# Kernel optimization log

Hardware: AMD Instinct MI355X
Metric: run time of the kernel (lower is better)

Reference implementation:

```python
import jax, jax.numpy as jnp
import numpy as np

BETA = 0.25
NUM_EMB = 8192
EMB_DIM = 256


def setup_inputs() -> dict:
    key = jax.random.key(0)
    k1, k2 = jax.random.split(key)
    z = jax.random.normal(k1, (32, 32, 32, EMB_DIM), dtype=jnp.float32)
    # codebook init: uniform in [-1/K, 1/K], stored as [D, K] like the TF layer
    embeddings = jax.random.uniform(
        k2, (EMB_DIM, NUM_EMB), dtype=jnp.float32,
        minval=-1.0 / NUM_EMB, maxval=1.0 / NUM_EMB)
    return {"z": z, "embeddings": embeddings}


def reference(z, embeddings):
    # inference path (training falsy): no EMA updates
    z_flat = z.reshape(-1, EMB_DIM)  # [N, D]
    # squared euclidean distances [N, K]
    distances = (jnp.sum(z_flat * z_flat, axis=1, keepdims=True)
                 + jnp.sum(embeddings * embeddings, axis=0)
                 - 2.0 * (z_flat @ embeddings))
    encoding_indices = jnp.argmin(distances, axis=1)  # [N] int
    quantized = embeddings.T[encoding_indices].reshape(z.shape)

    commitment_loss = BETA * jnp.mean((jax.lax.stop_gradient(quantized) - z) ** 2)
    # straight-through estimator
    quantized_st = z + jax.lax.stop_gradient(quantized - z)

    # avg one-hot probs via scatter-add (avoids materializing [N, K] one-hot)
    n_tokens = z_flat.shape[0]
    counts = jnp.zeros((NUM_EMB,), dtype=jnp.float32).at[encoding_indices].add(1.0)
    avg_probs = counts / n_tokens
    perplexity = jnp.exp(-jnp.sum(avg_probs * jnp.log(avg_probs + 1e-10)))

    return (quantized_st, encoding_indices, 0, commitment_loss, perplexity)
```

## Files before the change

### kernel.cpp

```cpp
#include <hip/hip_runtime.h>
#include <math.h>
#include <stdint.h>


#define N_TOK   32768
#define DIM     256
#define K_EMB   8192

#define WS_S       0
#define WS_E2      131072
#define WS_PVAL    163840
#define WS_PIDX    425984
#define WS_CNT     688128
#define WS_PART    720896
#define WS_ZT      851968
#define WS_END_ZT  34406400
#define WS_ET      34406400
#define WS_END_ET  42795008

__device__ __forceinline__ void gload_lds16(const float* g, float* l) {
  __builtin_amdgcn_global_load_lds(
      (const __attribute__((address_space(1))) void*)g,
      (__attribute__((address_space(3))) void*)l, 16, 0, 0);
}

__global__ void k_sumz(const float* __restrict__ z, float* __restrict__ S) {
  int t = blockIdx.x * blockDim.x + threadIdx.x;
  const float4* zp = (const float4*)(z + (size_t)t * DIM);
  float s = 0.0f;
  #pragma unroll 4
  for (int g = 0; g < DIM / 4; ++g) {
    float4 v = zp[g];
    s = __fadd_rn(s, __fmul_rn(v.x, v.x));
    s = __fadd_rn(s, __fmul_rn(v.y, v.y));
    s = __fadd_rn(s, __fmul_rn(v.z, v.z));
    s = __fadd_rn(s, __fmul_rn(v.w, v.w));
  }
  S[t] = s;
}

__global__ void k_sume(const float* __restrict__ E, float* __restrict__ e2) {
  __shared__ float part[4][64];
  int c  = threadIdx.x & 63;
  int dq = threadIdx.x >> 6;
  int col = blockIdx.x * 64 + c;
  float s = 0.0f;
  #pragma unroll 4
  for (int d = dq * 64; d < dq * 64 + 64; ++d) {
    float v = E[(size_t)d * K_EMB + col];
    s = __fadd_rn(s, __fmul_rn(v, v));
  }
  part[dq][c] = s;
  __syncthreads();
  if (threadIdx.x < 64)
    e2[blockIdx.x * 64 + threadIdx.x] =
        __fadd_rn(__fadd_rn(part[0][threadIdx.x], part[1][threadIdx.x]),
                  __fadd_rn(part[2][threadIdx.x], part[3][threadIdx.x]));
}

__global__ void k_transpose_z(const float* __restrict__ z, float* __restrict__ zT) {
  __shared__ float tile[32][33];
  int n0 = blockIdx.x * 32, d0 = blockIdx.y * 32;
  int lx = threadIdx.x, ly = threadIdx.y;
  #pragma unroll
  for (int r = 0; r < 32; r += 8)
    tile[ly + r][lx] = z[(size_t)(n0 + ly + r) * DIM + d0 + lx];
  __syncthreads();
  #pragma unroll
  for (int r = 0; r < 32; r += 8)
    zT[(size_t)(d0 + ly + r) * N_TOK + n0 + lx] = tile[lx][ly + r];
}

__global__ void k_transpose_e(const float* __restrict__ E, float* __restrict__ ET) {
  __shared__ float tile[32][33];
  int k0 = blockIdx.x * 32, d0 = blockIdx.y * 32;
  int lx = threadIdx.x, ly = threadIdx.y;
  #pragma unroll
  for (int r = 0; r < 32; r += 8)
    tile[ly + r][lx] = E[(size_t)(d0 + ly + r) * K_EMB + k0 + lx];
  __syncthreads();
  #pragma unroll
  for (int r = 0; r < 32; r += 8)
    ET[(size_t)(k0 + ly + r) * DIM + d0 + lx] = tile[lx][ly + r];
}

#define BM 128
#define BN 256
#define BK 16
#define KSTEPS 16
#define NCT 16
#define NSTEP (NCT * KSTEPS)

template<bool USE_ZT>
__launch_bounds__(256, 2)
__global__ void k_dist(const float* __restrict__ zsrc, const float* __restrict__ E,
                       const float* __restrict__ S, const float* __restrict__ e2,
                       float* __restrict__ pval, int* __restrict__ pidx) {
  __shared__ __align__(16) float smem[2 * BK * BM + 2 * BK * BN];
  float* zt = smem;
  float* et = smem + 2 * BK * BM;

  const int tid = threadIdx.x;
  const int tx  = tid & 15;
  const int ty  = tid >> 4;
  const int wv  = tid >> 6;
  const int ln  = tid & 63;
  const int rowblk = blockIdx.x >> 1;
  const int half   = blockIdx.x & 1;
  const int row0    = rowblk * BM;
  const int colbase = half * (NCT * BN);

  float acc[8][16];
  #pragma unroll
  for (int i = 0; i < 8; ++i)
    #pragma unroll
    for (int j = 0; j < 16; ++j) acc[i][j] = 0.0f;

  float best[8];
  int   bidx[8];
  #pragma unroll
  for (int i = 0; i < 8; ++i) { best[i] = 3.402823466e38f; bidx[i] = 0; }

  float Sreg[8];
  #pragma unroll
  for (int i = 0; i < 8; ++i)
    Sreg[i] = S[row0 + (i >> 2) * 64 + ty * 4 + (i & 3)];

  auto LOADE = [&](int gs) {
    int ks = gs & (KSTEPS - 1), ct = gs >> 4;
    const float* gsrc = E + (size_t)(ks * BK) * K_EMB + colbase + ct * BN + ln * 4;
    float* lb = et + (gs & 1) * (BK * BN);
    #pragma unroll
    for (int it = 0; it < 4; ++it) {
      int dd = it * 4 + wv;
      gload_lds16(gsrc + (size_t)dd * K_EMB, lb + dd * BN);
    }
  };
  auto LOADZT = [&](int gs) {
    int d0 = (gs & (KSTEPS - 1)) * BK;
    float* lb = zt + (gs & 1) * (BK * BM);
    int h = ln >> 5, j = ln & 31;
    #pragma unroll
    for (int it = 0; it < 2; ++it) {
      int p = it * 4 + wv;
      gload_lds16(zsrc + (size_t)(d0 + 2 * p + h) * N_TOK + row0 + j * 4,
                  lb + (2 * p) * BM);
    }
  };
  float4 pz[2];
  auto LOADZG = [&](int gs) {
    int d0 = (gs & (KSTEPS - 1)) * BK;
    #pragma unroll
    for (int it = 0; it < 2; ++it) {
      int l = it * 256 + tid;
      pz[it] = *(const float4*)&zsrc[(size_t)(row0 + (l >> 2)) * DIM + d0 + (l & 3) * 4];
    }
  };
  auto STOREZ = [&](int b) {
    float* zb = zt + b * (BK * BM);
    #pragma unroll
    for (int it = 0; it < 2; ++it) {
      int l = it * 256 + tid;
      int zrow = l >> 2, zdg = l & 3;
      zb[(zdg * 4 + 0) * BM + zrow] = pz[it].x;
      zb[(zdg * 4 + 1) * BM + zrow] = pz[it].y;
      zb[(zdg * 4 + 2) * BM + zrow] = pz[it].z;
      zb[(zdg * 4 + 3) * BM + zrow] = pz[it].w;
    }
  };

  LOADE(0);
  if (USE_ZT) { LOADZT(0); } else { LOADZG(0); STOREZ(0); }
  __syncthreads();

  for (int gs = 0; gs < NSTEP; ++gs) {
    const int buf = gs & 1;
    if (gs + 1 < NSTEP) {
      LOADE(gs + 1);
      if (USE_ZT) LOADZT(gs + 1); else LOADZG(gs + 1);
    }

    const float* zb = zt + buf * (BK * BM);
    const float* eb = et + buf * (BK * BN);
    #pragma unroll 4
    for (int d = 0; d < BK; ++d) {
      float zr[8], ec[16];
      {
        float4 a0 = *(const float4*)&zb[d * BM + ty * 4];
        float4 a1 = *(const float4*)&zb[d * BM + 64 + ty * 4];
        zr[0] = a0.x; zr[1] = a0.y; zr[2] = a0.z; zr[3] = a0.w;
        zr[4] = a1.x; zr[5] = a1.y; zr[6] = a1.z; zr[7] = a1.w;
      }
      #pragma unroll
      for (int g = 0; g < 4; ++g) {
        float4 w = *(const float4*)&eb[d * BN + g * 64 + tx * 4];
        ec[g * 4 + 0] = w.x; ec[g * 4 + 1] = w.y;
        ec[g * 4 + 2] = w.z; ec[g * 4 + 3] = w.w;
      }
      #pragma unroll
      for (int i = 0; i < 8; ++i)
        #pragma unroll
        for (int j = 0; j < 16; ++j)
          acc[i][j] = fmaf(zr[i], ec[j], acc[i][j]);
    }

    if ((gs & (KSTEPS - 1)) == KSTEPS - 1) {
      int col0c = colbase + (gs >> 4) * BN;
      float e2r[16];
      #pragma unroll
      for (int j = 0; j < 16; ++j)
        e2r[j] = e2[col0c + (j >> 2) * 64 + tx * 4 + (j & 3)];
      #pragma unroll
      for (int i = 0; i < 8; ++i) {
        #pragma unroll
        for (int j = 0; j < 16; ++j) {
          float t1  = __fadd_rn(Sreg[i], e2r[j]);
          float val = __fsub_rn(t1, __fmul_rn(2.0f, acc[i][j]));
          int cidx  = col0c + (j >> 2) * 64 + tx * 4 + (j & 3);
          if (val < best[i]) { best[i] = val; bidx[i] = cidx; }
          acc[i][j] = 0.0f;
        }
      }
    }

    if (!USE_ZT && gs + 1 < NSTEP) STOREZ(buf ^ 1);
    __syncthreads();
  }

  float* redv = smem;
  int*   redi = (int*)(smem + BM * 16);
  #pragma unroll
  for (int i = 0; i < 8; ++i) {
    int r = (i >> 2) * 64 + ty * 4 + (i & 3);
    redv[r * 16 + tx] = best[i];
    redi[r * 16 + tx] = bidx[i];
  }
  __syncthreads();
  if (tid < BM) {
    float bv = redv[tid * 16];
    int   bi = redi[tid * 16];
    #pragma unroll
    for (int u = 1; u < 16; ++u) {
      float v = redv[tid * 16 + u];
      int  ii = redi[tid * 16 + u];
      if (v < bv || (v == bv && ii < bi)) { bv = v; bi = ii; }
    }
    pval[(size_t)half * N_TOK + row0 + tid] = bv;
    pidx[(size_t)half * N_TOK + row0 + tid] = bi;
  }
}

__global__ void k_out(const float* __restrict__ z, const float* __restrict__ E,
                      const float* __restrict__ ET, int useET,
                      const float* __restrict__ pval, const int* __restrict__ pidx,
                      float* __restrict__ out, float* __restrict__ counts,
                      float* __restrict__ partials) {
  int n = blockIdx.x;
  int t = threadIdx.x;
  float bv = pval[n];
  int   bi = pidx[n];
  {
    float v = pval[(size_t)N_TOK + n];
    int  ii = pidx[(size_t)N_TOK + n];
    if (v < bv || (v == bv && ii < bi)) { bv = v; bi = ii; }
  }
  int idx = bi;

  float q  = useET ? ET[(size_t)idx * DIM + t]
                   : E[(size_t)t * K_EMB + idx];
  float zz = z[(size_t)n * DIM + t];
  float dd = __fsub_rn(q, zz);
  out[(size_t)n * DIM + t] = __fadd_rn(zz, dd);
  float sq = __fmul_rn(dd, dd);

  #pragma unroll
  for (int o = 32; o > 0; o >>= 1) sq += __shfl_down(sq, o);
  __shared__ float wsum[4];
  if ((t & 63) == 0) wsum[t >> 6] = sq;
  __syncthreads();
  if (t == 0) {
    partials[n] = ((wsum[0] + wsum[1]) + (wsum[2] + wsum[3]));
    atomicAdd(&counts[idx], 1.0f);
    out[(size_t)N_TOK * DIM + n] = (float)idx;
  }
}

__global__ void k_final(const float* __restrict__ partials,
                        const float* __restrict__ counts,
                        float* __restrict__ out) {
  __shared__ double sd[256];
  int t = threadIdx.x;
  double s = 0.0;
  for (int i = t; i < N_TOK; i += 256) s += (double)partials[i];
  sd[t] = s;
  __syncthreads();
  for (int o = 128; o > 0; o >>= 1) { if (t < o) sd[t] += sd[t + o]; __syncthreads(); }
  double totalLoss = sd[0];
  __syncthreads();
  double s2 = 0.0;
  for (int k = t; k < K_EMB; k += 256) {
    float p = counts[k] * (1.0f / (float)N_TOK);
    s2 += (double)(p * logf(p + 1e-10f));
  }
  sd[t] = s2;
  __syncthreads();
  for (int o = 128; o > 0; o >>= 1) { if (t < o) sd[t] += sd[t + o]; __syncthreads(); }
  if (t == 0) {
    const size_t base = (size_t)N_TOK * DIM + N_TOK;
    out[base + 0] = 0.0f;
    out[base + 1] = 0.25f * (float)(totalLoss / (double)(N_TOK * DIM));
    out[base + 2] = expf(-(float)sd[0]);
  }
}

extern "C" void kernel_launch(void* const* d_in, const int* in_sizes, int n_in,
                              void* d_out, int out_size, void* d_ws, size_t ws_size,
                              hipStream_t stream) {
  const float* z = (const float*)d_in[0];
  const float* E = (const float*)d_in[1];
  float* out = (float*)d_out;
  char* w = (char*)d_ws;
  float* S        = (float*)(w + WS_S);
  float* e2       = (float*)(w + WS_E2);
  float* pval     = (float*)(w + WS_PVAL);
  int*   pidx     = (int*)(w + WS_PIDX);
  float* counts   = (float*)(w + WS_CNT);
  float* partials = (float*)(w + WS_PART);
  float* zT       = (float*)(w + WS_ZT);
  float* ET       = (float*)(w + WS_ET);
  const int useZT = (ws_size >= (size_t)WS_END_ZT) ? 1 : 0;
  const int useET = (ws_size >= (size_t)WS_END_ET) ? 1 : 0;

  hipMemsetAsync(w + WS_CNT, 0, K_EMB * sizeof(float), stream);
  k_sumz<<<N_TOK / 256, 256, 0, stream>>>(z, S);
  k_sume<<<K_EMB / 64, 256, 0, stream>>>(E, e2);
  if (useZT)
    k_transpose_z<<<dim3(N_TOK / 32, DIM / 32), dim3(32, 8), 0, stream>>>(z, zT);
  if (useET)
    k_transpose_e<<<dim3(K_EMB / 32, DIM / 32), dim3(32, 8), 0, stream>>>(E, ET);
  if (useZT)
    k_dist<true><<<512, 256, 0, stream>>>(zT, E, S, e2, pval, pidx);
  else
    k_dist<false><<<512, 256, 0, stream>>>(z, E, S, e2, pval, pidx);
  k_out<<<N_TOK, 256, 0, stream>>>(z, E, ET, useET, pval, pidx, out, counts, partials);
  k_final<<<1, 256, 0, stream>>>(partials, counts, out);
}
```

Baseline: 1.690 ms.

## Read z rows directly into registers and use packed FMA in distance GEMM

Removes the z transpose kernel and the z tile in shared memory. Each thread now loads its 8 z rows straight from global memory as float4 into registers, and the inner product uses v_pk_fma_f32 on pairs of codebook columns. This cuts the transpose pass, the LDS traffic and the LDS footprint for z, and halves the FMA instruction count. In exchange every thread does redundant, uncoalesced global loads of z, since the 16 threads sharing a row each read it, with no prefetch for that stream, and the register-packed data adds pressure on a 2-blocks-per-CU launch bound.

```diff
diff --git a/kernel.cpp b/kernel.cpp
--- a/kernel.cpp
+++ b/kernel.cpp
@@ -13,10 +13,14 @@
 #define WS_PIDX    425984
 #define WS_CNT     688128
 #define WS_PART    720896
-#define WS_ZT      851968
-#define WS_END_ZT  34406400
-#define WS_ET      34406400
-#define WS_END_ET  42795008
+#define WS_ET      851968
+#define WS_END_ET  9240576
+
+typedef __attribute__((ext_vector_type(2))) float f32x2;
+
+__device__ __forceinline__ void pk_fma(f32x2& a, f32x2 x, f32x2 y) {
+  asm("v_pk_fma_f32 %0, %1, %2, %0" : "+v"(a) : "v"(x), "v"(y));
+}
 
 __device__ __forceinline__ void gload_lds16(const float* g, float* l) {
   __builtin_amdgcn_global_load_lds(
@@ -58,19 +62,6 @@
                   __fadd_rn(part[2][threadIdx.x], part[3][threadIdx.x]));
 }
 
-__global__ void k_transpose_z(const float* __restrict__ z, float* __restrict__ zT) {
-  __shared__ float tile[32][33];
-  int n0 = blockIdx.x * 32, d0 = blockIdx.y * 32;
-  int lx = threadIdx.x, ly = threadIdx.y;
-  #pragma unroll
-  for (int r = 0; r < 32; r += 8)
-    tile[ly + r][lx] = z[(size_t)(n0 + ly + r) * DIM + d0 + lx];
-  __syncthreads();
-  #pragma unroll
-  for (int r = 0; r < 32; r += 8)
-    zT[(size_t)(d0 + ly + r) * N_TOK + n0 + lx] = tile[lx][ly + r];
-}
-
 __global__ void k_transpose_e(const float* __restrict__ E, float* __restrict__ ET) {
   __shared__ float tile[32][33];
   int k0 = blockIdx.x * 32, d0 = blockIdx.y * 32;
@@ -91,14 +82,12 @@
 #define NCT 16
 #define NSTEP (NCT * KSTEPS)
 
-template<bool USE_ZT>
 __launch_bounds__(256, 2)
-__global__ void k_dist(const float* __restrict__ zsrc, const float* __restrict__ E,
+__global__ void k_dist(const float* __restrict__ z, const float* __restrict__ E,
                        const float* __restrict__ S, const float* __restrict__ e2,
                        float* __restrict__ pval, int* __restrict__ pidx) {
-  __shared__ __align__(16) float smem[2 * BK * BM + 2 * BK * BN];
-  float* zt = smem;
-  float* et = smem + 2 * BK * BM;
+  __shared__ __align__(16) float smem[2 * BK * BN];
+  float* et = smem;
 
   const int tid = threadIdx.x;
   const int tx  = tid & 15;
@@ -110,21 +99,25 @@
   const int row0    = rowblk * BM;
   const int colbase = half * (NCT * BN);
 
-  float acc[8][16];
+  f32x2 acc[8][8];
   #pragma unroll
   for (int i = 0; i < 8; ++i)
     #pragma unroll
-    for (int j = 0; j < 16; ++j) acc[i][j] = 0.0f;
+    for (int jp = 0; jp < 8; ++jp) acc[i][jp] = (f32x2){0.0f, 0.0f};
 
   float best[8];
   int   bidx[8];
   #pragma unroll
   for (int i = 0; i < 8; ++i) { best[i] = 3.402823466e38f; bidx[i] = 0; }
 
+  const float* zrow[8];
   float Sreg[8];
   #pragma unroll
-  for (int i = 0; i < 8; ++i)
-    Sreg[i] = S[row0 + (i >> 2) * 64 + ty * 4 + (i & 3)];
+  for (int i = 0; i < 8; ++i) {
+    int r = row0 + (i >> 2) * 64 + ty * 4 + (i & 3);
+    zrow[i] = z + (size_t)r * DIM;
+    Sreg[i] = S[r];
+  }
 
   auto LOADE = [&](int gs) {
     int ks = gs & (KSTEPS - 1), ct = gs >> 4;
@@ -136,72 +129,42 @@
       gload_lds16(gsrc + (size_t)dd * K_EMB, lb + dd * BN);
     }
   };
-  auto LOADZT = [&](int gs) {
-    int d0 = (gs & (KSTEPS - 1)) * BK;
-    float* lb = zt + (gs & 1) * (BK * BM);
-    int h = ln >> 5, j = ln & 31;
-    #pragma unroll
-    for (int it = 0; it < 2; ++it) {
-      int p = it * 4 + wv;
-      gload_lds16(zsrc + (size_t)(d0 + 2 * p + h) * N_TOK + row0 + j * 4,
-                  lb + (2 * p) * BM);
-    }
-  };
-  float4 pz[2];
-  auto LOADZG = [&](int gs) {
-    int d0 = (gs & (KSTEPS - 1)) * BK;
-    #pragma unroll
-    for (int it = 0; it < 2; ++it) {
-      int l = it * 256 + tid;
-      pz[it] = *(const float4*)&zsrc[(size_t)(row0 + (l >> 2)) * DIM + d0 + (l & 3) * 4];
-    }
-  };
-  auto STOREZ = [&](int b) {
-    float* zb = zt + b * (BK * BM);
-    #pragma unroll
-    for (int it = 0; it < 2; ++it) {
-      int l = it * 256 + tid;
-      int zrow = l >> 2, zdg = l & 3;
-      zb[(zdg * 4 + 0) * BM + zrow] = pz[it].x;
-      zb[(zdg * 4 + 1) * BM + zrow] = pz[it].y;
-      zb[(zdg * 4 + 2) * BM + zrow] = pz[it].z;
-      zb[(zdg * 4 + 3) * BM + zrow] = pz[it].w;
-    }
-  };
 
   LOADE(0);
-  if (USE_ZT) { LOADZT(0); } else { LOADZG(0); STOREZ(0); }
   __syncthreads();
 
   for (int gs = 0; gs < NSTEP; ++gs) {
     const int buf = gs & 1;
-    if (gs + 1 < NSTEP) {
-      LOADE(gs + 1);
-      if (USE_ZT) LOADZT(gs + 1); else LOADZG(gs + 1);
-    }
-
-    const float* zb = zt + buf * (BK * BM);
+    if (gs + 1 < NSTEP) LOADE(gs + 1);
+
     const float* eb = et + buf * (BK * BN);
-    #pragma unroll 4
-    for (int d = 0; d < BK; ++d) {
-      float zr[8], ec[16];
-      {
-        float4 a0 = *(const float4*)&zb[d * BM + ty * 4];
-        float4 a1 = *(const float4*)&zb[d * BM + 64 + ty * 4];
-        zr[0] = a0.x; zr[1] = a0.y; zr[2] = a0.z; zr[3] = a0.w;
-        zr[4] = a1.x; zr[5] = a1.y; zr[6] = a1.z; zr[7] = a1.w;
-      }
-      #pragma unroll
-      for (int g = 0; g < 4; ++g) {
-        float4 w = *(const float4*)&eb[d * BN + g * 64 + tx * 4];
-        ec[g * 4 + 0] = w.x; ec[g * 4 + 1] = w.y;
-        ec[g * 4 + 2] = w.z; ec[g * 4 + 3] = w.w;
-      }
+    const int d0 = (gs & (KSTEPS - 1)) * BK;
+
+    #pragma unroll
+    for (int dq = 0; dq < 4; ++dq) {
+      float4 zv[8];
       #pragma unroll
       for (int i = 0; i < 8; ++i)
+        zv[i] = *(const float4*)(zrow[i] + d0 + dq * 4);
+      #pragma unroll
+      for (int t = 0; t < 4; ++t) {
+        int d = dq * 4 + t;
+        f32x2 ep[8];
         #pragma unroll
-        for (int j = 0; j < 16; ++j)
-          acc[i][j] = fmaf(zr[i], ec[j], acc[i][j]);
+        for (int g = 0; g < 4; ++g) {
+          float4 w = *(const float4*)&eb[d * BN + g * 64 + tx * 4];
+          ep[2 * g + 0] = (f32x2){w.x, w.y};
+          ep[2 * g + 1] = (f32x2){w.z, w.w};
+        }
+        #pragma unroll
+        for (int i = 0; i < 8; ++i) {
+          float zs = (t == 0) ? zv[i].x : (t == 1) ? zv[i].y
+                   : (t == 2) ? zv[i].z : zv[i].w;
+          f32x2 zp = (f32x2){zs, zs};
+          #pragma unroll
+          for (int jp = 0; jp < 8; ++jp) pk_fma(acc[i][jp], zp, ep[jp]);
+        }
+      }
     }
 
     if ((gs & (KSTEPS - 1)) == KSTEPS - 1) {
@@ -214,16 +177,16 @@
       for (int i = 0; i < 8; ++i) {
         #pragma unroll
         for (int j = 0; j < 16; ++j) {
-          float t1  = __fadd_rn(Sreg[i], e2r[j]);
-          float val = __fsub_rn(t1, __fmul_rn(2.0f, acc[i][j]));
-          int cidx  = col0c + (j >> 2) * 64 + tx * 4 + (j & 3);
+          float dotv = acc[i][j >> 1][j & 1];
+          float t1   = __fadd_rn(Sreg[i], e2r[j]);
+          float val  = __fsub_rn(t1, __fmul_rn(2.0f, dotv));
+          int cidx   = col0c + (j >> 2) * 64 + tx * 4 + (j & 3);
           if (val < best[i]) { best[i] = val; bidx[i] = cidx; }
-          acc[i][j] = 0.0f;
+          acc[i][j >> 1][j & 1] = 0.0f;
         }
       }
     }
 
-    if (!USE_ZT && gs + 1 < NSTEP) STOREZ(buf ^ 1);
     __syncthreads();
   }
 
@@ -326,22 +289,15 @@
   int*   pidx     = (int*)(w + WS_PIDX);
   float* counts   = (float*)(w + WS_CNT);
   float* partials = (float*)(w + WS_PART);
-  float* zT       = (float*)(w + WS_ZT);
   float* ET       = (float*)(w + WS_ET);
-  const int useZT = (ws_size >= (size_t)WS_END_ZT) ? 1 : 0;
   const int useET = (ws_size >= (size_t)WS_END_ET) ? 1 : 0;
 
   hipMemsetAsync(w + WS_CNT, 0, K_EMB * sizeof(float), stream);
   k_sumz<<<N_TOK / 256, 256, 0, stream>>>(z, S);
   k_sume<<<K_EMB / 64, 256, 0, stream>>>(E, e2);
-  if (useZT)
-    k_transpose_z<<<dim3(N_TOK / 32, DIM / 32), dim3(32, 8), 0, stream>>>(z, zT);
   if (useET)
     k_transpose_e<<<dim3(K_EMB / 32, DIM / 32), dim3(32, 8), 0, stream>>>(E, ET);
-  if (useZT)
-    k_dist<true><<<512, 256, 0, stream>>>(zT, E, S, e2, pval, pidx);
-  else
-    k_dist<false><<<512, 256, 0, stream>>>(z, E, S, e2, pval, pidx);
+  k_dist<<<512, 256, 0, stream>>>(z, E, S, e2, pval, pidx);
   k_out<<<N_TOK, 256, 0, stream>>>(z, E, ET, useET, pval, pidx, out, counts, partials);
   k_final<<<1, 256, 0, stream>>>(partials, counts, out);
 }
```

After: 1.849 ms. 1.09x slower.
